# Kernel optimization log

Hardware: AMD Instinct MI355X
Metric: run time of the kernel (lower is better)

## Reference

```python
import jax, jax.numpy as jnp
import numpy as np

N, C, T, V = 32, 64, 256, 25   # batch, channels, frames, joints
REL, OUT, K = 8, 64, 5         # rel_channels = C//8, out_channels, 5 topology branches
NU = 17                        # upper-body joints (lower = V - NU = 8)


def setup_inputs() -> dict:
    key = jax.random.key(0)
    ks = jax.random.split(key, 8)
    sC = np.float32(1.0 / np.sqrt(C))
    sR = np.float32(1.0 / np.sqrt(REL))
    return {
        "x": jax.random.normal(ks[0], (N, C, T, V), jnp.float32),
        "A": jax.random.uniform(ks[1], (K, V, V), jnp.float32),
        # stacked 1x1-conv weights for the 5 branches (conv{k}_1_1, _1_2, _2, _3, _4)
        "W11": jax.random.normal(ks[2], (K, REL, C), jnp.float32) * sC,
        "b11": jnp.zeros((K, REL), jnp.float32),
        "W12": jax.random.normal(ks[3], (K, REL, C), jnp.float32) * sC,
        "b12": jnp.zeros((K, REL), jnp.float32),
        "W2": jax.random.normal(ks[4], (K, REL, C), jnp.float32) * sC,
        "b2": jnp.zeros((K, REL), jnp.float32),
        "W3": jax.random.normal(ks[5], (K, OUT, C), jnp.float32) * sC,
        "b3": jnp.zeros((K, OUT), jnp.float32),
        "W4": jax.random.normal(ks[6], (K, OUT, REL), jnp.float32) * sR,
        "b4": jnp.zeros((K, OUT), jnp.float32),
    }


def reference(x, A, W11, b11, W12, b12, W2, b2, W3, b3, W4, b4):
    # 1x1 conv followed by mean over T commutes with the (linear) conv:
    # conv(x).mean(T) == W @ x.mean(T) + b. Pool once, reuse across branches.
    mu = jnp.mean(x[:, :, :, :NU], axis=2)   # (N, C, 17)
    ml = jnp.mean(x[:, :, :, NU:], axis=2)   # (N, C, 8)

    u11 = jnp.einsum('krc,ncv->knrv', W11, mu) + b11[:, None, :, None]  # (K,N,R,17)
    u2 = jnp.einsum('krc,ncv->knrv', W2, mu) + b2[:, None, :, None]     # (K,N,R,17)
    l12 = jnp.einsum('krc,ncv->knrv', W12, ml) + b12[:, None, :, None]  # (K,N,R,8)
    l2 = jnp.einsum('krc,ncv->knrv', W2, ml) + b2[:, None, :, None]     # (K,N,R,8)

    # pairwise-difference topology blocks
    x_a = jnp.tanh(u11[..., :, None] - u2[..., None, :])   # (K,N,R,17,17)
    x_b = jnp.tanh(u11[..., :, None] - l2[..., None, :])   # (K,N,R,17,8)
    x_c = jnp.tanh(l12[..., :, None] - u2[..., None, :])   # (K,N,R,8,17)
    x_d = jnp.tanh(l12[..., :, None] - l2[..., None, :])   # (K,N,R,8,8)

    up = jnp.concatenate([x_a, x_b], axis=-1)   # (K,N,R,17,25)
    lo = jnp.concatenate([x_c, x_d], axis=-1)   # (K,N,R,8,25)

    # the original rotates the upper blocks: branch k uses upper from branch (k+1)%5
    up_rot = jnp.concatenate([up[1:], up[:1]], axis=0)
    full = jnp.concatenate([up_rot, lo], axis=-2)  # (K,N,R,25,25)

    graphs = jnp.einsum('kor,knruv->knouv', W4, full) + b4[:, None, :, None, None]  # (K,N,O,25,25)

    alpha = jnp.ones((K,), jnp.float32)  # default branch scales
    g = graphs * alpha[:, None, None, None, None] + A[:, None, None, :, :]

    x2 = jnp.einsum('koc,nctv->knotv', W3, x) + b3[:, None, :, None, None]  # (K,N,O,T,25)
    out = jnp.einsum('knouv,knotv->notu', g, x2)  # summed over the 5 branches
    return out, graphs
```

## Files before the change

kernel.cpp:

```cpp
#include <hip/hip_runtime.h>
#include <cstdint>
#include <cstddef>

#define N_  32
#define C_  64
#define T_  256
#define V_  25
#define R_  8
#define O_  64
#define K_  5
#define NU_ 17
#define U_  25
#define CV  (C_ * V_)
#define OG  2
#define NB  (OG * 32)

#define OUT_ELEMS ((size_t)N_ * O_ * T_ * V_)

typedef __attribute__((ext_vector_type(8))) short bf16x8;
typedef __attribute__((ext_vector_type(4))) float f32x4;

static __device__ __forceinline__ unsigned short f2bf(float f) {
    union { float f; unsigned u; } c; c.f = f;
    return (unsigned short)((c.u + 0x8000u) >> 16);
}
static __device__ __forceinline__ float bf2f(unsigned short h) {
    union { unsigned u; float f; } c; c.u = ((unsigned)h) << 16; return c.f;
}
static __device__ __forceinline__ float bf_lo(unsigned d) {
    union { unsigned u; float f; } c; c.u = d << 16; return c.f;
}
static __device__ __forceinline__ float bf_hi(unsigned d) {
    union { unsigned u; float f; } c; c.u = d & 0xFFFF0000u; return c.f;
}
static __device__ __forceinline__ unsigned pk2(float a, float b) {
    union { float f; unsigned u; } ca, cb; ca.f = a; cb.f = b;
    return ((ca.u + 0x8000u) >> 16) | ((cb.u + 0x8000u) & 0xFFFF0000u);
}
static __device__ __forceinline__ unsigned cvtpk(float a, float b) {
    unsigned r;
    asm("v_cvt_pk_bf16_f32 %0, %1, %2" : "=v"(r) : "v"(a), "v"(b));
    return r;
}

__global__ void k_xcast(const float* __restrict__ x, unsigned short* __restrict__ xT3,
                        float* __restrict__ pp) {
    __shared__ unsigned short tile[C_][408];
    int bid = blockIdx.x;
    int n = bid >> 4, tb = bid & 15;
    int tid = threadIdx.x;
    const float* xb = x + (size_t)n * C_ * T_ * V_ + tb * 400;
#pragma unroll
    for (int it = 0; it < 25; ++it) {
        int i = it * 256 + tid;
        int c = i / 100, q = i - c * 100;
        float4 v4 = *(const float4*)(xb + (size_t)c * (T_ * V_) + q * 4);
        uint2 w;
        w.x = pk2(v4.x, v4.y);
        w.y = pk2(v4.z, v4.w);
        *(uint2*)&tile[c][q * 4] = w;
    }
    __syncthreads();
    unsigned short* dstb = xT3 + ((size_t)(n * 16 + tb) * 200) * 128;
    for (int i = tid; i < 200 * 16; i += 256) {
        int sp = i >> 4, tl = i & 15;
        int v = sp >> 3, c0 = (sp & 7) * 8;
        unsigned short h[8];
#pragma unroll
        for (int j = 0; j < 8; ++j) h[j] = tile[c0 + j][tl * 25 + v];
        uint4 pk;
        pk.x = (unsigned)h[0] | ((unsigned)h[1] << 16);
        pk.y = (unsigned)h[2] | ((unsigned)h[3] << 16);
        pk.z = (unsigned)h[4] | ((unsigned)h[5] << 16);
        pk.w = (unsigned)h[6] | ((unsigned)h[7] << 16);
        *(uint4*)(dstb + (size_t)sp * 128 + tl * 8) = pk;
    }
    float* ppd = pp + ((size_t)n * 16 + tb) * CV;
    for (int e = tid; e < CV; e += 256) {
        int c = e / 25, v = e - c * 25;
        float s = 0.f;
#pragma unroll
        for (int t = 0; t < 16; ++t) s += bf2f(tile[c][t * 25 + v]);
        ppd[e] = s;
    }
}

__global__ void k_pool(const float* __restrict__ x, float* __restrict__ pool) {
    int nc = blockIdx.x;
    int t  = threadIdx.x;
    const float* px = x + ((size_t)nc * T_ + t) * V_;
    float acc[V_];
#pragma unroll
    for (int v = 0; v < V_; ++v) acc[v] = px[v];
#pragma unroll
    for (int off = 32; off > 0; off >>= 1) {
#pragma unroll
        for (int v = 0; v < V_; ++v) acc[v] += __shfl_down(acc[v], off, 64);
    }
    __shared__ float sm[4][V_];
    int wave = t >> 6, lane = t & 63;
    if (lane == 0) {
#pragma unroll
        for (int v = 0; v < V_; ++v) sm[wave][v] = acc[v];
    }
    __syncthreads();
    if (t < V_) {
        float s = sm[0][t] + sm[1][t] + sm[2][t] + sm[3][t];
        pool[(size_t)nc * V_ + t] = s * (1.0f / T_);
    }
}

__global__ void k_tvals(const float* __restrict__ pool,
                        const float* __restrict__ W11, const float* __restrict__ b11,
                        const float* __restrict__ W12, const float* __restrict__ b12,
                        const float* __restrict__ W2,  const float* __restrict__ b2,
                        float* __restrict__ t2o, float* __restrict__ tSo) {
    int kn = blockIdx.x;
    int k = kn / N_, n = kn % N_;
    int tid = threadIdx.x;
    int r = tid >> 5, v = tid & 31;
    if (v >= V_) return;
    const float* pp = pool + (size_t)n * C_ * V_ + v;
    const float* w2 = W2 + ((size_t)k * R_ + r) * C_;
    const float* w1 = ((v < NU_) ? W11 : W12) + ((size_t)k * R_ + r) * C_;
    float a2 = b2[k * R_ + r];
    float a1 = (v < NU_) ? b11[k * R_ + r] : b12[k * R_ + r];
    for (int c = 0; c < C_; ++c) {
        float p = pp[(size_t)c * V_];
        a2 += w2[c] * p;
        a1 += w1[c] * p;
    }
    size_t idx = (((size_t)k * N_ + n) * R_ + r) * V_ + v;
    t2o[idx] = a2;
    tSo[idx] = a1;
}

__global__ void k_graphs(const float* __restrict__ t2v, const float* __restrict__ tSv,
                         const float* __restrict__ W4, const float* __restrict__ b4,
                         float* __restrict__ graphs) {
    int kn = blockIdx.x;
    int k = kn / N_, n = kn % N_;
    int kup = (k + 1) % K_;
    __shared__ float F[R_][V_ * V_];
    __shared__ float w4s[O_][R_];
    __shared__ float b4s[O_];
    int tid = threadIdx.x;
    for (int i = tid; i < O_ * R_; i += 256) w4s[i / R_][i % R_] = W4[(size_t)k * O_ * R_ + i];
    if (tid < O_) b4s[tid] = b4[k * O_ + tid];
    for (int idx = tid; idx < R_ * V_ * V_; idx += 256) {
        int r = idx / (V_ * V_), uv = idx % (V_ * V_);
        int u = uv / V_, v = uv % V_;
        int ks = (u < NU_) ? kup : k;
        size_t base = (((size_t)ks * N_ + n) * R_ + r) * V_;
        F[r][uv] = tanhf(tSv[base + u] - t2v[base + v]);
    }
    __syncthreads();
    float* gout = graphs + ((size_t)k * N_ + n) * O_ * (V_ * V_);
    for (int idx = tid; idx < O_ * V_ * V_; idx += 256) {
        int o = idx / (V_ * V_), uv = idx % (V_ * V_);
        float a = b4s[o];
#pragma unroll
        for (int r = 0; r < R_; ++r) a += w4s[o][r] * F[r][uv];
        gout[idx] = a;
    }
}

__global__ void k_graphs2c(const float* __restrict__ pp,
                           const float* __restrict__ W11, const float* __restrict__ b11,
                           const float* __restrict__ W12, const float* __restrict__ b12,
                           const float* __restrict__ W2,  const float* __restrict__ b2,
                           const float* __restrict__ W4,  const float* __restrict__ b4,
                           float* __restrict__ graphs) {
    int bid = blockIdx.x;
    int og = bid & 1;
    int kn = bid >> 1;
    int k = kn / N_, n = kn % N_;
    int kup = (k + 1) % K_;
    __shared__ float poolL[CV];
    __shared__ float t2s[2][R_][V_];
    __shared__ float tSs[2][R_][V_];
    __shared__ float F[R_][V_ * V_];
    __shared__ float w4s[O_][R_];
    __shared__ float b4s[O_];
    int tid = threadIdx.x;
    for (int i = tid; i < O_ * R_; i += 512) w4s[i / R_][i % R_] = W4[(size_t)k * O_ * R_ + i];
    if (tid < O_) b4s[tid] = b4[k * O_ + tid];
    const float* ppn = pp + (size_t)n * 16 * CV;
    for (int i = tid; i < CV; i += 512) {
        float s = 0.f;
#pragma unroll
        for (int tb = 0; tb < 16; ++tb) s += ppn[(size_t)tb * CV + i];
        poolL[i] = s * (1.0f / T_);
    }
    __syncthreads();
    for (int i = tid; i < 2 * R_ * V_; i += 512) {
        int ks = i / (R_ * V_);
        int rem = i - ks * (R_ * V_);
        int r = rem / V_, v = rem - r * V_;
        int kk = ks ? kup : k;
        const float* w2 = W2 + ((size_t)kk * R_ + r) * C_;
        const float* w1 = ((v < NU_) ? W11 : W12) + ((size_t)kk * R_ + r) * C_;
        float a2 = b2[kk * R_ + r];
        float a1 = (v < NU_) ? b11[kk * R_ + r] : b12[kk * R_ + r];
        for (int c = 0; c < C_; ++c) {
            float p = poolL[c * 25 + v];
            a2 += w2[c] * p;
            a1 += w1[c] * p;
        }
        t2s[ks][r][v] = a2;
        tSs[ks][r][v] = a1;
    }
    __syncthreads();
    for (int idx = tid; idx < R_ * V_ * V_; idx += 512) {
        int r = idx / (V_ * V_), uv = idx % (V_ * V_);
        int u = uv / V_, v = uv % V_;
        int ks = (u < NU_) ? 1 : 0;
        F[r][uv] = tanhf(tSs[ks][r][u] - t2s[ks][r][v]);
    }
    __syncthreads();
    float* gout = graphs + ((size_t)k * N_ + n) * O_ * (V_ * V_);
    const int half = O_ * V_ * V_ / 2;
    for (int idx = og * half + tid; idx < (og + 1) * half; idx += 512) {
        int o = idx / (V_ * V_), uv = idx % (V_ * V_);
        float a = b4s[o];
#pragma unroll
        for (int r = 0; r < R_; ++r) a += w4s[o][r] * F[r][uv];
        gout[idx] = a;
    }
}

__global__ __launch_bounds__(256, 4) void k_main_fast(
    const unsigned short* __restrict__ xT3,
    const float* __restrict__ graphs,
    const float* __restrict__ Adj,
    const float* __restrict__ W3,
    const float* __restrict__ b3,
    float* __restrict__ out) {

    __shared__ unsigned short Hs[4][4][NB][8];
    __shared__ uint2 Gbf4[OG * 625];
    __shared__ unsigned short Gbf1[OG * 625];
    __shared__ unsigned short W3kmh[K_ * OG * C_];
    __shared__ float biasS[NB];

    const int tid = threadIdx.x;
    int bid = blockIdx.x;
    bid = (bid & 7) * 128 + (bid >> 3);
    const int obase = (bid & 31) * OG;
    const int n = bid >> 5;
    const int lane = tid & 63;
    const int wv_ = tid >> 6;

    const size_t kstride = (size_t)N_ * O_ * 625;
    for (int i = tid; i < OG * 625; i += 256) {
        int o = i / 625, uv = i - o * 625;
        int u = uv / 25, v = uv - u * 25;
        size_t gb = ((size_t)n * O_ + obase + o) * 625 + uv;
        float g0 = graphs[gb]               + Adj[uv];
        float g1 = graphs[gb + kstride]     + Adj[625 + uv];
        float g2 = graphs[gb + 2 * kstride] + Adj[1250 + uv];
        float g3 = graphs[gb + 3 * kstride] + Adj[1875 + uv];
        float g4 = graphs[gb + 4 * kstride] + Adj[2500 + uv];
        int idx = o * 625 + v * 25 + u;
        uint2 w; w.x = pk2(g0, g1); w.y = pk2(g2, g3);
        Gbf4[idx] = w;
        Gbf1[idx] = f2bf(g4);
    }
    for (int i = tid; i < K_ * OG * C_; i += 256) {
        int k = i / (OG * C_);
        int rem = i - k * (OG * C_);
        int o = rem >> 6, c = rem & 63;
        W3kmh[(k * OG + o) * C_ + c] = f2bf(W3[((size_t)k * O_ + obase + o) * C_ + c]);
    }
    __syncthreads();

    if (tid < NB) {
        int o = tid >> 5, u = tid & 31;
        float bv = 0.f;
        if (u < U_) {
            float s0 = 0.f, s1 = 0.f, s2 = 0.f, s3 = 0.f, s4 = 0.f;
            for (int v = 0; v < V_; ++v) {
                int idx = o * 625 + v * 25 + u;
                uint2 w = Gbf4[idx];
                s0 += bf_lo(w.x); s1 += bf_hi(w.x);
                s2 += bf_lo(w.y); s3 += bf_hi(w.y);
                s4 += bf2f(Gbf1[idx]);
            }
            bv = s0 * b3[0 * O_ + obase + o] + s1 * b3[1 * O_ + obase + o]
               + s2 * b3[2 * O_ + obase + o] + s3 * b3[3 * O_ + obase + o]
               + s4 * b3[4 * O_ + obase + o];
        }
        biasS[tid] = bv;
    }

    const int sl = wv_;
    const int hncol = lane;
    const int ho = hncol >> 5;
    const int hu = hncol & 31;
    const uint2* gp4 = &Gbf4[ho * 625 + hu];
    const unsigned short* gp1 = &Gbf1[ho * 625 + hu];
    const unsigned short* wbh = &W3kmh[ho * C_ + sl * 8];
    char* hwb = (char*)&Hs[0][sl][hncol][0];

    auto h_form = [&](char* hwp, const int parOff , f32x4 g, float g5) {
        float gk[5] = {g[0], g[1], g[2], g[3], g5};
        float h0 = 0.f, h1 = 0.f, h2 = 0.f, h3 = 0.f;
        float h4 = 0.f, h5 = 0.f, h6 = 0.f, h7 = 0.f;
#pragma unroll
        for (int k = 0; k < K_; ++k) {
            uint4 wk = *(const uint4*)(wbh + parOff + k * (OG * C_));
            float gv_ = gk[k];
            h0 += bf_lo(wk.x) * gv_; h1 += bf_hi(wk.x) * gv_;
            h2 += bf_lo(wk.y) * gv_; h3 += bf_hi(wk.y) * gv_;
            h4 += bf_lo(wk.z) * gv_; h5 += bf_hi(wk.z) * gv_;
            h6 += bf_lo(wk.w) * gv_; h7 += bf_hi(wk.w) * gv_;
        }
        uint4 hv;
        hv.x = cvtpk(h0, h1); hv.y = cvtpk(h2, h3);
        hv.z = cvtpk(h4, h5); hv.w = cvtpk(h6, h7);
        *(uint4*)hwp = hv;
    };
    auto ld_g = [&](int voff25, f32x4& g, float& g5) {
        if (hu < U_) {
            uint2 gw = gp4[voff25];
            g[0] = bf_lo(gw.x); g[1] = bf_hi(gw.x);
            g[2] = bf_lo(gw.y); g[3] = bf_hi(gw.y);
            g5 = bf2f(gp1[voff25]);
        } else { g = (f32x4){0.f, 0.f, 0.f, 0.f}; g5 = 0.f; }
    };

    const int wm = wv_;
    const int lr = lane & 15;
    const int eg = lane >> 4;

    f32x4 acc[4][4];
#pragma unroll
    for (int mt = 0; mt < 4; ++mt)
#pragma unroll
        for (int nt = 0; nt < 4; ++nt) acc[mt][nt] = (f32x4){0.f, 0.f, 0.f, 0.f};

    const unsigned short* An = xT3 + (size_t)n * (T_ * CV);
    const unsigned short* a0 = An + ((size_t)((wm * 4 + 0) * 200 + eg)) * 128 + lr * 8;
    const unsigned short* a1 = a0 + 200 * 128;
    const unsigned short* a2 = a0 + 400 * 128;
    const unsigned short* a3 = a0 + 600 * 128;
    const char* hrb = (const char*)&Hs[0][eg][lr][0];

    auto consume = [&](int sub , int bufb ) {
        uint4 av0 = *(const uint4*)(a0 + sub);
        uint4 av1 = *(const uint4*)(a1 + sub);
        uint4 av2 = *(const uint4*)(a2 + sub);
        uint4 av3 = *(const uint4*)(a3 + sub);
        bf16x8 b[4];
#pragma unroll
        for (int nt = 0; nt < 4; ++nt)
            b[nt] = *(const bf16x8*)(hrb + bufb + nt * 256);
        __builtin_amdgcn_s_setprio(1);
        union { uint4 u; bf16x8 h; } c0, c1, c2, c3;
        c0.u = av0; c1.u = av1; c2.u = av2; c3.u = av3;
#pragma unroll
        for (int nt = 0; nt < 4; ++nt) acc[0][nt] = __builtin_amdgcn_mfma_f32_16x16x32_bf16(c0.h, b[nt], acc[0][nt], 0, 0, 0);
#pragma unroll
        for (int nt = 0; nt < 4; ++nt) acc[1][nt] = __builtin_amdgcn_mfma_f32_16x16x32_bf16(c1.h, b[nt], acc[1][nt], 0, 0, 0);
#pragma unroll
        for (int nt = 0; nt < 4; ++nt) acc[2][nt] = __builtin_amdgcn_mfma_f32_16x16x32_bf16(c2.h, b[nt], acc[2][nt], 0, 0, 0);
#pragma unroll
        for (int nt = 0; nt < 4; ++nt) acc[3][nt] = __builtin_amdgcn_mfma_f32_16x16x32_bf16(c3.h, b[nt], acc[3][nt], 0, 0, 0);
        __builtin_amdgcn_s_setprio(0);
    };

    f32x4 gv; float gv5;
    ld_g(0, gv, gv5);
    h_form(hwb, 0, gv, gv5);
    h_form(hwb + 4096, 32, gv, gv5);
    __syncthreads();

    for (int kc2 = 0; kc2 < 25; ++kc2) {
        const int rb = (kc2 & 1) * 8192;
        const int wb = 8192 - rb;
        if (kc2 + 1 < 25) ld_g((kc2 + 1) * 25, gv, gv5);
        consume(0, rb);
        consume(512, rb + 4096);
        if (kc2 + 1 < 25) {
            h_form(hwb + wb, 0, gv, gv5);
            h_form(hwb + wb + 4096, 32, gv, gv5);
        }
        __syncthreads();
        a0 += 1024; a1 += 1024; a2 += 1024; a3 += 1024;
    }

#pragma unroll
    for (int nt = 0; nt < 4; ++nt) {
        int ncol = nt * 16 + lr;
        int ol = ncol >> 5;
        int u  = ncol & 31;
        if (u < U_) {
            float bv = biasS[ncol];
            float* ob = out + ((size_t)n * O_ + obase + ol) * T_ * V_ + u;
#pragma unroll
            for (int mt = 0; mt < 4; ++mt) {
                int t0 = wm * 64 + mt * 16 + eg * 4;
#pragma unroll
                for (int r2 = 0; r2 < 4; ++r2)
                    ob[(size_t)(t0 + r2) * V_] = acc[mt][nt][r2] + bv;
            }
        }
    }
}

#define OB 4
#define TB 64
__global__ __launch_bounds__(256, 1) void k_main_slow(
    const float* __restrict__ x, const float* __restrict__ graphs,
    const float* __restrict__ A, const float* __restrict__ W3,
    const float* __restrict__ b3, float* __restrict__ out) {
    int bid = blockIdx.x;
    int tb = bid & 3;
    int ob = (bid >> 2) & 15;
    int n  = bid >> 6;
    int tid = threadIdx.x;
    int ol = tid >> 6;
    int tl = tid & 63;
    int t = tb * TB + tl;
    int o = ob * OB + ol;

    __shared__ float Gs[K_][OB][V_][28];
    __shared__ float W3s[K_][OB][C_];
    __shared__ float b3s[K_][OB];

    for (int i = tid; i < K_ * OB * V_ * V_; i += 256) {
        int k   = i / (OB * V_ * V_);
        int rem = i % (OB * V_ * V_);
        int oo  = rem / (V_ * V_);
        int uv  = rem % (V_ * V_);
        Gs[k][oo][uv / V_][uv % V_] =
            graphs[(((size_t)k * N_ + n) * O_ + ob * OB + oo) * (V_ * V_) + uv]
            + A[k * V_ * V_ + uv];
    }
    for (int i = tid; i < K_ * OB * C_; i += 256) {
        int k   = i / (OB * C_);
        int rem = i % (OB * C_);
        int oo  = rem / C_, c = rem % C_;
        W3s[k][oo][c] = W3[((size_t)k * O_ + ob * OB + oo) * C_ + c];
    }
    if (tid < K_ * OB) b3s[tid / OB][tid % OB] = b3[(tid / OB) * O_ + ob * OB + tid % OB];
    __syncthreads();

    float x2[K_][V_];
#pragma unroll
    for (int k = 0; k < K_; ++k)
#pragma unroll
        for (int v = 0; v < V_; ++v) x2[k][v] = b3s[k][ol];

    const float* xb = x + ((size_t)n * C_ * T_ + t) * V_;
    for (int c = 0; c < C_; ++c) {
        const float* p = xb + (size_t)c * T_ * V_;
        float xv[V_];
#pragma unroll
        for (int v = 0; v < V_; ++v) xv[v] = p[v];
#pragma unroll
        for (int k = 0; k < K_; ++k) {
            float w = W3s[k][ol][c];
#pragma unroll
            for (int v = 0; v < V_; ++v) x2[k][v] += w * xv[v];
        }
    }

    float acc[V_];
#pragma unroll
    for (int u = 0; u < V_; ++u) acc[u] = 0.0f;
#pragma unroll
    for (int k = 0; k < K_; ++k) {
#pragma unroll
        for (int u = 0; u < V_; ++u) {
            const float* gr = &Gs[k][ol][u][0];
            float s = 0.0f;
#pragma unroll
            for (int v = 0; v < V_; ++v) s += gr[v] * x2[k][v];
            acc[u] += s;
        }
    }
    float* po = out + (((size_t)n * O_ + o) * T_ + t) * V_;
#pragma unroll
    for (int u = 0; u < V_; ++u) po[u] = acc[u];
}

extern "C" void kernel_launch(void* const* d_in, const int* in_sizes, int n_in,
                              void* d_out, int out_size, void* d_ws, size_t ws_size,
                              hipStream_t stream) {
    const float* x   = (const float*)d_in[0];
    const float* A   = (const float*)d_in[1];
    const float* W11 = (const float*)d_in[2];
    const float* b11 = (const float*)d_in[3];
    const float* W12 = (const float*)d_in[4];
    const float* b12 = (const float*)d_in[5];
    const float* W2  = (const float*)d_in[6];
    const float* b2  = (const float*)d_in[7];
    const float* W3  = (const float*)d_in[8];
    const float* b3  = (const float*)d_in[9];
    const float* W4  = (const float*)d_in[10];
    const float* b4  = (const float*)d_in[11];

    float* out    = (float*)d_out;
    float* graphs = out + OUT_ELEMS;

    const size_t xT_bytes = sizeof(unsigned short) * (size_t)N_ * T_ * CV;
    const size_t pp_bytes = sizeof(float) * (size_t)N_ * 16 * CV;
    const size_t hdr      = (size_t)(1 << 20);
    const bool fast = (ws_size >= hdr + xT_bytes + pp_bytes);

    const size_t poolElems = (size_t)N_ * C_ * V_;
    const size_t tElems    = (size_t)K_ * N_ * R_ * V_;
    const size_t slowNeed  = (poolElems + 2 * tElems) * sizeof(float);

    float* scratch = (fast || ws_size >= slowNeed) ? (float*)d_ws : out;
    float* pool = scratch;
    float* t2v  = scratch + poolElems;
    float* tSv  = t2v + tElems;
    unsigned short* xT3 = (unsigned short*)((char*)d_ws + hdr);
    float* pp = (float*)((char*)d_ws + hdr + xT_bytes);

    if (fast) {
        k_xcast   <<<N_ * 16, 256, 0, stream>>>(x, xT3, pp);
        k_graphs2c<<<K_ * N_ * 2, 512, 0, stream>>>(pp, W11, b11, W12, b12, W2, b2, W4, b4, graphs);
        k_main_fast<<<N_ * 32, 256, 0, stream>>>(xT3, graphs, A, W3, b3, out);
    } else {
        k_pool  <<<N_ * C_, 256, 0, stream>>>(x, pool);
        k_tvals <<<K_ * N_, 256, 0, stream>>>(pool, W11, b11, W12, b12, W2, b2, t2v, tSv);
        k_graphs<<<K_ * N_, 256, 0, stream>>>(t2v, tSv, W4, b4, graphs);
        k_main_slow<<<N_ * (O_ / OB) * 4, 256, 0, stream>>>(x, graphs, A, W3, b3, out);
    }
}
```

Measured before the change: 109.4 us.

## Refactor main GEMM: compute per-branch x2 tiles via MFMA, then contract with prepacked graph fragments

Adds a new tiered path. The graph-producing kernel now also writes bf16 (graph+A) fragments laid out for MFMA, and a bias kernel folds b3 through the summed graphs into an extra column. The main kernel first computes the small W3·x projection for 5 branches × 2 outputs into swizzled LDS, then runs a single K=128 MFMA contraction over (k,v), replacing the old per-column H formation. It adds a memset, an extra launch and extra workspace traffic, and it halves occupancy.

```diff
diff --git a/kernel.cpp b/kernel.cpp
--- a/kernel.cpp
+++ b/kernel.cpp
@@ -41,6 +41,9 @@
     unsigned r;
     asm("v_cvt_pk_bf16_f32 %0, %1, %2" : "=v"(r) : "v"(a), "v"(b));
     return r;
+}
+static __device__ __forceinline__ bf16x8 asbf(uint4 u) {
+    union { uint4 u; bf16x8 h; } c; c.u = u; return c.h;
 }
 
 __global__ void k_xcast(const float* __restrict__ x, unsigned short* __restrict__ xT3,
@@ -165,12 +168,14 @@
     }
 }
 
-__global__ void k_graphs2c(const float* __restrict__ pp,
+__global__ void k_graphs2f(const float* __restrict__ pp,
                            const float* __restrict__ W11, const float* __restrict__ b11,
                            const float* __restrict__ W12, const float* __restrict__ b12,
                            const float* __restrict__ W2,  const float* __restrict__ b2,
                            const float* __restrict__ W4,  const float* __restrict__ b4,
-                           float* __restrict__ graphs) {
+                           const float* __restrict__ Adj,
+                           float* __restrict__ graphs,
+                           unsigned short* __restrict__ gfrag) {
     int bid = blockIdx.x;
     int og = bid & 1;
     int kn = bid >> 1;
@@ -226,10 +231,154 @@
 #pragma unroll
         for (int r = 0; r < R_; ++r) a += w4s[o][r] * F[r][uv];
         gout[idx] = a;
-    }
-}
-
-__global__ __launch_bounds__(256, 4) void k_main_fast(
+        if (gfrag) {
+            int u = uv / 25, v = uv - u * 25;
+            gfrag[(((size_t)n * 64 + o) * 32 + u) * 128 + k * 25 + v] =
+                f2bf(a + Adj[k * 625 + uv]);
+        }
+    }
+}
+
+__global__ void k_biasf(const float* __restrict__ graphs, const float* __restrict__ Adj,
+                        const float* __restrict__ b3, unsigned short* __restrict__ gfrag) {
+    int bid = blockIdx.x;
+    int n = bid >> 3, og8 = bid & 7;
+    int ol = threadIdx.x >> 5, u = threadIdx.x & 31;
+    int o = og8 * 8 + ol;
+    if (u >= U_) return;
+    float s = 0.f;
+    for (int k = 0; k < K_; ++k) {
+        const float* gp = graphs + (((size_t)k * N_ + n) * O_ + o) * 625 + u * 25;
+        const float* ap = Adj + k * 625 + u * 25;
+        float t = 0.f;
+#pragma unroll
+        for (int v = 0; v < V_; ++v) t += gp[v] + ap[v];
+        s += t * b3[k * O_ + o];
+    }
+    gfrag[(((size_t)n * 64 + o) * 32 + u) * 128 + 125] = f2bf(s);
+}
+
+__global__ __launch_bounds__(256, 2) void k_main_fac(
+    const unsigned short* __restrict__ xT3,
+    const unsigned short* __restrict__ gfrag,
+    const float* __restrict__ W3,
+    float* __restrict__ out) {
+
+    __shared__ float x2f[2 * 64 * 128];
+
+    const int tid = threadIdx.x;
+    int raw = blockIdx.x;
+    int bid = (raw & 7) * 512 + (raw >> 3);
+    const int og = bid & 31;
+    const int tb = (bid >> 5) & 3;
+    const int n  = bid >> 7;
+    const int obase = og * 2;
+    const int tgb = tb * 64;
+    const int lane = tid & 63;
+    const int w = tid >> 6;
+    const int lr = lane & 15;
+    const int eg = lane >> 4;
+
+    {
+        f32x4 z = {0.f, 0.f, 0.f, 0.f};
+        for (int i = tid; i < 2 * 64 * 128 / 4; i += 256) ((f32x4*)x2f)[i] = z;
+    }
+    __syncthreads();
+    if (tid < 128) {
+        int o = tid >> 6, t = tid & 63;
+        x2f[o * 8192 + t * 128 + (125 ^ ((t & 6) << 2))] = 1.0f;
+    }
+
+    bf16x8 wb0, wb1;
+    {
+        short h0[8] = {0,0,0,0,0,0,0,0}, h1[8] = {0,0,0,0,0,0,0,0};
+        if (lr < 10) {
+            int k = lr >> 1, o = lr & 1;
+            const float* wp = W3 + ((size_t)k * O_ + obase + o) * C_;
+#pragma unroll
+            for (int e = 0; e < 8; ++e) {
+                h0[e] = (short)f2bf(wp[eg * 8 + e]);
+                h1[e] = (short)f2bf(wp[32 + eg * 8 + e]);
+            }
+        }
+        wb0 = (bf16x8){h0[0], h0[1], h0[2], h0[3], h0[4], h0[5], h0[6], h0[7]};
+        wb1 = (bf16x8){h1[0], h1[1], h1[2], h1[3], h1[4], h1[5], h1[6], h1[7]};
+    }
+
+    {
+        const int ttb = tb * 4 + w;
+        const unsigned short* pA = xT3 + (size_t)n * (T_ * CV)
+                                 + ((size_t)(ttb * 200) + eg) * 128 + lr * 8;
+        const int kA = lr >> 1, oA = lr & 1;
+        const int tl0 = w * 16 + eg * 4;
+        for (int v = 0; v < 25; ++v) {
+            uint4 a0 = *(const uint4*)(pA + v * 1024);
+            uint4 a1 = *(const uint4*)(pA + v * 1024 + 512);
+            f32x4 d = {0.f, 0.f, 0.f, 0.f};
+            d = __builtin_amdgcn_mfma_f32_16x16x32_bf16(asbf(a0), wb0, d, 0, 0, 0);
+            d = __builtin_amdgcn_mfma_f32_16x16x32_bf16(asbf(a1), wb1, d, 0, 0, 0);
+            if (lr < 10) {
+                int kv = kA * 25 + v;
+#pragma unroll
+                for (int r2 = 0; r2 < 4; ++r2) {
+                    int t = tl0 + r2;
+                    x2f[oA * 8192 + t * 128 + (kv ^ ((t & 6) << 2))] = d[r2];
+                }
+            }
+        }
+    }
+    __syncthreads();
+
+    f32x4 acc[2][2];
+#pragma unroll
+    for (int o = 0; o < 2; ++o)
+#pragma unroll
+        for (int nt = 0; nt < 2; ++nt) acc[o][nt] = (f32x4){0.f, 0.f, 0.f, 0.f};
+
+    const unsigned short* gb = gfrag + (((size_t)n * 64 + obase) * 32) * 128;
+    const int tB = w * 16 + lr;
+    const int swB = (tB & 6) << 2;
+#pragma unroll
+    for (int o = 0; o < 2; ++o) {
+        uint4 bf[2][4];
+#pragma unroll
+        for (int nt = 0; nt < 2; ++nt)
+#pragma unroll
+            for (int ks = 0; ks < 4; ++ks)
+                bf[nt][ks] = *(const uint4*)(gb + (size_t)o * 4096
+                                             + (nt * 16 + lr) * 128 + ks * 32 + eg * 8);
+#pragma unroll
+        for (int ks = 0; ks < 4; ++ks) {
+            int base = o * 8192 + tB * 128 + ((ks * 32 + eg * 8) ^ swB);
+            f32x4 x0 = *(const f32x4*)&x2f[base];
+            f32x4 x1 = *(const f32x4*)&x2f[base + 4];
+            uint4 au;
+            au.x = cvtpk(x0[0], x0[1]); au.y = cvtpk(x0[2], x0[3]);
+            au.z = cvtpk(x1[0], x1[1]); au.w = cvtpk(x1[2], x1[3]);
+            bf16x8 af = asbf(au);
+            acc[o][0] = __builtin_amdgcn_mfma_f32_16x16x32_bf16(af, asbf(bf[0][ks]), acc[o][0], 0, 0, 0);
+            acc[o][1] = __builtin_amdgcn_mfma_f32_16x16x32_bf16(af, asbf(bf[1][ks]), acc[o][1], 0, 0, 0);
+        }
+    }
+
+#pragma unroll
+    for (int o = 0; o < 2; ++o) {
+        float* ob = out + ((size_t)n * O_ + obase + o) * T_ * V_;
+#pragma unroll
+        for (int nt = 0; nt < 2; ++nt) {
+            int u = nt * 16 + lr;
+            if (u < U_) {
+#pragma unroll
+                for (int r2 = 0; r2 < 4; ++r2) {
+                    int t = tgb + w * 16 + eg * 4 + r2;
+                    ob[(size_t)t * V_ + u] = acc[o][nt][r2];
+                }
+            }
+        }
+    }
+}
+
+__global__ __launch_bounds__(256, 4) void k_main_fast2(
     const unsigned short* __restrict__ xT3,
     const float* __restrict__ graphs,
     const float* __restrict__ Adj,
@@ -302,7 +451,7 @@
     const unsigned short* wbh = &W3kmh[ho * C_ + sl * 8];
     char* hwb = (char*)&Hs[0][sl][hncol][0];
 
-    auto h_form = [&](char* hwp, const int parOff , f32x4 g, float g5) {
+    auto h_form = [&](char* hwp, const int parOff, f32x4 g, float g5) {
         float gk[5] = {g[0], g[1], g[2], g[3], g5};
         float h0 = 0.f, h1 = 0.f, h2 = 0.f, h3 = 0.f;
         float h4 = 0.f, h5 = 0.f, h6 = 0.f, h7 = 0.f;
@@ -346,7 +495,7 @@
     const unsigned short* a3 = a0 + 600 * 128;
     const char* hrb = (const char*)&Hs[0][eg][lr][0];
 
-    auto consume = [&](int sub , int bufb ) {
+    auto consume = [&](int sub, int bufb) {
         uint4 av0 = *(const uint4*)(a0 + sub);
         uint4 av1 = *(const uint4*)(a1 + sub);
         uint4 av2 = *(const uint4*)(a2 + sub);
@@ -506,24 +655,33 @@
 
     const size_t xT_bytes = sizeof(unsigned short) * (size_t)N_ * T_ * CV;
     const size_t pp_bytes = sizeof(float) * (size_t)N_ * 16 * CV;
+    const size_t gf_bytes = sizeof(unsigned short) * (size_t)N_ * 64 * 32 * 128;
     const size_t hdr      = (size_t)(1 << 20);
-    const bool fast = (ws_size >= hdr + xT_bytes + pp_bytes);
+    const bool tier1 = (ws_size >= hdr + xT_bytes + pp_bytes + gf_bytes);
+    const bool tier2 = (ws_size >= hdr + xT_bytes + pp_bytes);
 
     const size_t poolElems = (size_t)N_ * C_ * V_;
     const size_t tElems    = (size_t)K_ * N_ * R_ * V_;
     const size_t slowNeed  = (poolElems + 2 * tElems) * sizeof(float);
 
-    float* scratch = (fast || ws_size >= slowNeed) ? (float*)d_ws : out;
+    float* scratch = (tier2 || ws_size >= slowNeed) ? (float*)d_ws : out;
     float* pool = scratch;
     float* t2v  = scratch + poolElems;
     float* tSv  = t2v + tElems;
     unsigned short* xT3 = (unsigned short*)((char*)d_ws + hdr);
     float* pp = (float*)((char*)d_ws + hdr + xT_bytes);
-
-    if (fast) {
-        k_xcast   <<<N_ * 16, 256, 0, stream>>>(x, xT3, pp);
-        k_graphs2c<<<K_ * N_ * 2, 512, 0, stream>>>(pp, W11, b11, W12, b12, W2, b2, W4, b4, graphs);
-        k_main_fast<<<N_ * 32, 256, 0, stream>>>(xT3, graphs, A, W3, b3, out);
+    unsigned short* gfrag = (unsigned short*)((char*)d_ws + hdr + xT_bytes + pp_bytes);
+
+    if (tier1) {
+        k_xcast<<<N_ * 16, 256, 0, stream>>>(x, xT3, pp);
+        hipMemsetAsync(gfrag, 0, gf_bytes, stream);
+        k_graphs2f<<<K_ * N_ * 2, 512, 0, stream>>>(pp, W11, b11, W12, b12, W2, b2, W4, b4, A, graphs, gfrag);
+        k_biasf<<<N_ * 8, 256, 0, stream>>>(graphs, A, b3, gfrag);
+        k_main_fac<<<N_ * 4 * 32, 256, 0, stream>>>(xT3, gfrag, W3, out);
+    } else if (tier2) {
+        k_xcast<<<N_ * 16, 256, 0, stream>>>(x, xT3, pp);
+        k_graphs2f<<<K_ * N_ * 2, 512, 0, stream>>>(pp, W11, b11, W12, b12, W2, b2, W4, b4, A, graphs, (unsigned short*)nullptr);
+        k_main_fast2<<<N_ * 32, 256, 0, stream>>>(xT3, graphs, A, W3, b3, out);
     } else {
         k_pool  <<<N_ * C_, 256, 0, stream>>>(x, pool);
         k_tvals <<<K_ * N_, 256, 0, stream>>>(pool, W11, b11, W12, b12, W2, b2, t2v, tSv);
```

Result: slower. 163.6 us (+49.6%).
